# Kernel optimization log

Measured on AMD Instinct MI355X. Metric: run time of the kernel, lower is better.

## Reference

```python
import jax, jax.numpy as jnp
import numpy as np

B, S, H, HEADS = 4, 2048, 512, 8
DK = H // HEADS
LN_EPS = 1e-5
NEG_INF = -1e30


def setup_inputs() -> dict:
    key = jax.random.key(0)
    k = jax.random.split(key, 6)
    x = jax.random.normal(k[0], (B, S, H), dtype=jnp.float32)
    mask = jax.random.randint(k[1], (B, S), 0, 2, dtype=jnp.int32)
    # per-head Q/K/V projection weights stacked: [heads, H, dk]
    Wq = jax.random.normal(k[2], (HEADS, H, DK), dtype=jnp.float32) * 0.05
    Wk = jax.random.normal(k[3], (HEADS, H, DK), dtype=jnp.float32) * 0.05
    Wv = jax.random.normal(k[4], (HEADS, H, DK), dtype=jnp.float32) * 0.05
    # output projection: [heads*dk, H] (y = h @ Wo)
    Wo = jax.random.normal(k[5], (HEADS * DK, H), dtype=jnp.float32) * 0.05
    gamma = jnp.ones((H,), dtype=jnp.float32)
    beta = jnp.zeros((H,), dtype=jnp.float32)
    return {"x": x, "mask": mask, "Wq": Wq, "Wk": Wk, "Wv": Wv,
            "Wo": Wo, "gamma": gamma, "beta": beta}


def reference(x, mask, Wq, Wk, Wv, Wo, gamma, beta):
    # LayerNorm over hidden dim
    mu = jnp.mean(x, axis=-1, keepdims=True)
    var = jnp.mean(jnp.square(x - mu), axis=-1, keepdims=True)
    xn = (x - mu) * jax.lax.rsqrt(var + LN_EPS) * gamma + beta  # [B,S,H]

    mf = mask.astype(jnp.float32)  # [B,S]

    # batched per-head projections (original loops over heads)
    q = jnp.einsum('bsh,nhd->bnsd', xn, Wq)  # [B,heads,S,dk]
    kk = jnp.einsum('bsh,nhd->bnsd', xn, Wk)
    v = jnp.einsum('bsh,nhd->bnsd', xn, Wv)

    scores = jnp.einsum('bnqd,bnkd->bnqk', q, kk) / np.sqrt(DK).astype(np.float32)
    m = mf[:, None, None, :]  # [B,1,1,S] broadcast over query dim
    logits = m * scores + (1.0 - m) * NEG_INF
    probs = jax.nn.softmax(logits, axis=-1)
    attn = jnp.einsum('bnqk,bnkd->bnqd', probs, v)  # [B,heads,S,dk]

    h = attn.transpose(0, 2, 1, 3).reshape(x.shape[0], x.shape[1], HEADS * DK)
    out = h @ Wo + xn          # residual adds post-norm x (as in original)
    out = out * mf[:, :, None]  # zero out masked positions
    return out
```

## Files before the change

kernel.cpp:

```cpp
#include <hip/hip_runtime.h>
#include <hip/hip_bf16.h>
#include <math.h>

#define B_ 4
#define S_ 2048
#define H_ 512
#define HEADS_ 8
#define DK_ 64
#define NROWS_ (B_*S_)
#define LN_EPS_ 1e-5f
#define NEG_INF_ -1e30f
#define QSCALE_ (0.125f * 1.44269504088896f)

typedef short s8v __attribute__((ext_vector_type(8)));
typedef short s4v __attribute__((ext_vector_type(4)));
typedef float f4v __attribute__((ext_vector_type(4)));

typedef __attribute__((address_space(1))) unsigned int gu32_t;
typedef __attribute__((address_space(3))) unsigned int lu32_t;

__device__ __forceinline__ unsigned short f2bf(float f) {
    unsigned int u = __float_as_uint(f);
    u += 0x7FFFu + ((u >> 16) & 1u);
    return (unsigned short)(u >> 16);
}

__device__ __forceinline__ float bf2f(unsigned short u) {
    return __uint_as_float((unsigned int)u << 16);
}

__device__ __forceinline__ s4v pk4bf(float a, float b, float c, float d) {
    union { __hip_bfloat162 h[2]; s4v v; } u;
    u.h[0] = __float22bfloat162_rn(float2{a, b});
    u.h[1] = __float22bfloat162_rn(float2{c, d});
    return u.v;
}

__global__ __launch_bounds__(256) void prep_kernel(
        const float* __restrict__ x, const float* __restrict__ gamma,
        const float* __restrict__ beta, const int* __restrict__ mask,
        const float* __restrict__ Wq, const float* __restrict__ Wk,
        const float* __restrict__ Wv, const float* __restrict__ Wo,
        unsigned short* __restrict__ xnb, float* __restrict__ mb,
        unsigned short* __restrict__ Wt) {
    int bx = blockIdx.x;
    if (bx < 2048) {
        int row  = bx * 4 + (threadIdx.x >> 6);
        int lane = threadIdx.x & 63;
        const float4* xr = (const float4*)(x + (size_t)row * H_ + lane * 8);
        float4 a = xr[0], d = xr[1];
        float s  = (a.x + a.y) + (a.z + a.w) + (d.x + d.y) + (d.z + d.w);
        float ss = (a.x*a.x + a.y*a.y) + (a.z*a.z + a.w*a.w)
                 + (d.x*d.x + d.y*d.y) + (d.z*d.z + d.w*d.w);
        #pragma unroll
        for (int i = 1; i < 64; i <<= 1) {
            s  += __shfl_xor(s, i, 64);
            ss += __shfl_xor(ss, i, 64);
        }
        float mu  = s * (1.f / 512.f);
        float var = ss * (1.f / 512.f) - mu * mu;
        float rstd = rsqrtf(var + LN_EPS_);
        if (lane == 0) mb[row] = mask[row] ? 0.f : NEG_INF_;
        const float4* gp = (const float4*)(gamma + lane * 8);
        const float4* bp = (const float4*)(beta + lane * 8);
        float4 g0 = gp[0], g1 = gp[1], b0 = bp[0], b1 = bp[1];
        float4 y0, y1;
        y0.x = (a.x - mu) * rstd * g0.x + b0.x;
        y0.y = (a.y - mu) * rstd * g0.y + b0.y;
        y0.z = (a.z - mu) * rstd * g0.z + b0.z;
        y0.w = (a.w - mu) * rstd * g0.w + b0.w;
        y1.x = (d.x - mu) * rstd * g1.x + b1.x;
        y1.y = (d.y - mu) * rstd * g1.y + b1.y;
        y1.z = (d.z - mu) * rstd * g1.z + b1.z;
        y1.w = (d.w - mu) * rstd * g1.w + b1.w;
        union { s4v h[2]; s8v v; } pk;
        pk.h[0] = pk4bf(y0.x, y0.y, y0.z, y0.w);
        pk.h[1] = pk4bf(y1.x, y1.y, y1.z, y1.w);
        *(s8v*)(xnb + (size_t)row * H_ + lane * 8) = pk.v;
    } else {
        __shared__ float tile[32][33];
        int wid = bx - 2048;
        const float* src;
        int ld, drow, k0, c0;
        float scale = 1.f;
        if (wid < 768) {
            int z = wid >> 5, rem = wid & 31;
            int cx = rem & 1, ky = rem >> 1;
            k0 = ky * 32; c0 = cx * 32;
            int zw = z >> 3, head = z & 7;
            const float* W = (zw == 0) ? Wq : (zw == 1) ? Wk : Wv;
            if (zw == 0) scale = QSCALE_;
            src = W + (size_t)head * H_ * DK_;
            ld = DK_;
            drow = zw * 512 + head * 64;
        } else {
            int rem = wid - 768;
            int cx = rem & 15, ky = rem >> 4;
            k0 = ky * 32; c0 = cx * 32;
            src = Wo; ld = H_; drow = 1536;
        }
        int tx = threadIdx.x & 31, ty = threadIdx.x >> 5;
        #pragma unroll
        for (int i = 0; i < 4; i++)
            tile[ty * 4 + i][tx] = src[(size_t)(k0 + ty * 4 + i) * ld + c0 + tx];
        __syncthreads();
        #pragma unroll
        for (int i = 0; i < 4; i++) {
            int cc = ty * 4 + i;
            Wt[(size_t)(drow + c0 + cc) * 512 + k0 + tx] = f2bf(tile[tx][cc] * scale);
        }
    }
}

__device__ __forceinline__ void gemm_tile(
        const unsigned short* __restrict__ A,
        const unsigned short* __restrict__ Bt,
        int r0, int j0, f4v acc[4][4]) {
    __shared__ unsigned short As[2 * 128 * 32];
    __shared__ unsigned short Bs[2 * 128 * 32];
    int t = threadIdx.x;
    int wv = t >> 6, L = t & 63, c = L & 15, g = L >> 4;
    int m_base = (wv & 1) * 64, n_base = (wv >> 1) * 64;
    #pragma unroll
    for (int i = 0; i < 4; i++)
        #pragma unroll
        for (int j = 0; j < 4; j++) acc[i][j] = (f4v){0.f, 0.f, 0.f, 0.f};
    for (int k0 = 0; k0 < 512; k0 += 64) {
        __syncthreads();
        #pragma unroll
        for (int half = 0; half < 2; half++) {
            #pragma unroll
            for (int i = 0; i < 2; i++) {
                int u = wv * 128 + i * 64 + L;
                int row = u >> 2, k16 = u & 3;
                __builtin_amdgcn_global_load_lds(
                    (const gu32_t*)(A + (size_t)(r0 + row) * 512 + k0 + half * 32 + k16 * 8),
                    (lu32_t*)(As + half * 4096 + (size_t)(wv * 128 + i * 64) * 8), 16, 0, 0);
                __builtin_amdgcn_global_load_lds(
                    (const gu32_t*)(Bt + (size_t)(j0 + row) * 512 + k0 + half * 32 + k16 * 8),
                    (lu32_t*)(Bs + half * 4096 + (size_t)(wv * 128 + i * 64) * 8), 16, 0, 0);
            }
        }
        __asm__ volatile("s_waitcnt vmcnt(0)" ::: "memory");
        __syncthreads();
        #pragma unroll
        for (int half = 0; half < 2; half++) {
            s8v a[4], b[4];
            #pragma unroll
            for (int i = 0; i < 4; i++)
                a[i] = *(const s8v*)(As + half * 4096 + (size_t)(m_base + i * 16 + c) * 32 + g * 8);
            #pragma unroll
            for (int j = 0; j < 4; j++)
                b[j] = *(const s8v*)(Bs + half * 4096 + (size_t)(n_base + j * 16 + c) * 32 + g * 8);
            #pragma unroll
            for (int i = 0; i < 4; i++)
                #pragma unroll
                for (int j = 0; j < 4; j++)
                    acc[i][j] = __builtin_amdgcn_mfma_f32_16x16x32_bf16(
                        a[i], b[j], acc[i][j], 0, 0, 0);
        }
    }
}

__global__ __launch_bounds__(256) void qkv_gemm(
        const unsigned short* __restrict__ xnb,
        const unsigned short* __restrict__ Wt,
        unsigned short* __restrict__ Qb, unsigned short* __restrict__ Kf,
        unsigned short* __restrict__ Vf) {
    f4v acc[4][4];
    int t = threadIdx.x;
    int wv = t >> 6, L = t & 63, c = L & 15, g = L >> 4;
    int rb = wv & 1, cb = wv >> 1;
    if (blockIdx.x < 8) {
        int m0 = blockIdx.x * 128, n0 = blockIdx.y * 128;
        gemm_tile(Wt, xnb, m0, n0, acc);
        int R0 = m0 + rb * 64;
        int C0 = n0 + cb * 64;
        int hd = (R0 >> 6) & 7;
        int b  = C0 >> 11, srow0 = C0 & 2047;
        size_t bhbase = (size_t)(b * HEADS_ + hd) * S_ * DK_;
        if (R0 < 512) {
            #pragma unroll
            for (int msub = 0; msub < 4; msub++) {
                int dk4 = msub * 16 + g * 4;
                #pragma unroll
                for (int nsub = 0; nsub < 4; nsub++) {
                    int tok = srow0 + nsub * 16 + c;
                    s4v v = pk4bf(acc[msub][nsub][0], acc[msub][nsub][1],
                                  acc[msub][nsub][2], acc[msub][nsub][3]);
                    *(s4v*)(Qb + bhbase + (size_t)tok * DK_ + dk4) = v;
                }
            }
        } else {
            unsigned short* dst = Kf + bhbase + (size_t)(srow0 >> 6) * 4096;
            #pragma unroll
            for (int msub = 0; msub < 4; msub++) {
                int gx = (msub & 1) * 2 + (g >> 1);
                int slotbase = (g & 1) * 4 + (msub >> 1) * 8;
                #pragma unroll
                for (int nsub = 0; nsub < 4; nsub++) {
                    s4v v = pk4bf(acc[msub][nsub][0], acc[msub][nsub][1],
                                  acc[msub][nsub][2], acc[msub][nsub][3]);
                    *(s4v*)(dst + nsub * 1024 + (gx * 16 + c) * 16 + slotbase) = v;
                }
            }
        }
    } else {
        int r0 = blockIdx.y * 128, j0 = 1024 + (blockIdx.x - 8) * 128;
        gemm_tile(xnb, Wt, r0, j0, acc);
        int R0 = r0 + rb * 64;
        int C0 = j0 + cb * 64;
        int hd = (C0 >> 6) & 7;
        int b = R0 >> 11, srow0 = R0 & 2047;
        unsigned short* dst = Vf + (size_t)(b * HEADS_ + hd) * S_ * DK_
                              + (size_t)(srow0 >> 6) * 4096;
        #pragma unroll
        for (int msub = 0; msub < 4; msub++)
            #pragma unroll
            for (int nsub = 0; nsub < 4; nsub++) {
                s4v v = pk4bf(acc[msub][nsub][0], acc[msub][nsub][1],
                              acc[msub][nsub][2], acc[msub][nsub][3]);
                *(s4v*)(dst + nsub * 1024 + (g * 16 + c) * 16 + msub * 4) = v;
            }
    }
}

struct KHalf {
    s8v k0lo, k0hi, k1lo, k1hi;
    float4 mb0, mb1;
};

__global__ __launch_bounds__(256, 3) void attn_kernel(
        const unsigned short* __restrict__ Qb,
        const unsigned short* __restrict__ Kf,
        const unsigned short* __restrict__ Vf,
        const float* __restrict__ mb,
        unsigned short* __restrict__ hb) {
    __shared__ float red[2][64][2][17];

    int wv   = threadIdx.x >> 6;
    int qsub = wv & 1;
    int kp   = wv >> 1;
    int L  = threadIdx.x & 63;
    int c  = L & 15;
    int g  = L >> 4;

    unsigned wgid = blockIdx.x + blockIdx.y * 32u;
    unsigned xcd  = wgid & 7u;
    unsigned idx  = wgid >> 3;
    int bh = (int)(xcd + (idx >> 5) * 8u);
    int qt = (int)(idx & 31u);
    int b  = bh >> 3, n = bh & 7;
    int q0 = qt * 64 + qsub * 32;

    const unsigned short* Qbase = Qb + (size_t)bh * S_ * DK_;
    const unsigned short* Kp = Kf + (size_t)bh * S_ * DK_ + (size_t)kp * 16 * 4096 + L * 16;
    const unsigned short* Vp = Vf + (size_t)bh * S_ * DK_ + (size_t)kp * 16 * 4096 + L * 16;
    const float* mbrow = mb + b * S_ + kp * 1024;

    s8v qfA0 = *(const s8v*)(Qbase + (size_t)(q0 + c) * DK_ + g * 8);
    s8v qfA1 = *(const s8v*)(Qbase + (size_t)(q0 + c) * DK_ + 32 + g * 8);
    s8v qfB0 = *(const s8v*)(Qbase + (size_t)(q0 + 16 + c) * DK_ + g * 8);
    s8v qfB1 = *(const s8v*)(Qbase + (size_t)(q0 + 16 + c) * DK_ + 32 + g * 8);

    f4v accA[4], accB[4];
    #pragma unroll
    for (int i = 0; i < 4; i++) {
        accA[i] = (f4v){0.f, 0.f, 0.f, 0.f};
        accB[i] = (f4v){0.f, 0.f, 0.f, 0.f};
    }
    float lacA[4] = {0.f, 0.f, 0.f, 0.f};
    float lacB[4] = {0.f, 0.f, 0.f, 0.f};

    auto load_kh = [&](int kb, int h, KHalf& d) {
        const unsigned short* Kn = Kp + (size_t)kb * 4096;
        d.k0lo = *(const s8v*)(Kn + (h * 2 + 0) * 1024);
        d.k0hi = *(const s8v*)(Kn + (h * 2 + 0) * 1024 + 8);
        d.k1lo = *(const s8v*)(Kn + (h * 2 + 1) * 1024);
        d.k1hi = *(const s8v*)(Kn + (h * 2 + 1) * 1024 + 8);
        d.mb0  = *(const float4*)(mbrow + kb * 64 + h * 32 + g * 4);
        d.mb1  = *(const float4*)(mbrow + kb * 64 + h * 32 + 16 + g * 4);
    };

    auto compute_half = [&](const KHalf& d, int kb, int h) {
        const unsigned short* Vn = Vp + (size_t)kb * 4096;
        s8v vv[4];
        #pragma unroll
        for (int ds = 0; ds < 4; ds++)
            vv[ds] = *(const s8v*)(Vn + ds * 1024 + h * 8);
        f4v bias0 = (f4v){d.mb0.x, d.mb0.y, d.mb0.z, d.mb0.w};
        f4v bias1 = (f4v){d.mb1.x, d.mb1.y, d.mb1.z, d.mb1.w};
        f4v sA0 = bias0, sA1 = bias1, sB0 = bias0, sB1 = bias1;
        sA0 = __builtin_amdgcn_mfma_f32_16x16x32_bf16(d.k0lo, qfA0, sA0, 0, 0, 0);
        sA0 = __builtin_amdgcn_mfma_f32_16x16x32_bf16(d.k0hi, qfA1, sA0, 0, 0, 0);
        sA1 = __builtin_amdgcn_mfma_f32_16x16x32_bf16(d.k1lo, qfA0, sA1, 0, 0, 0);
        sA1 = __builtin_amdgcn_mfma_f32_16x16x32_bf16(d.k1hi, qfA1, sA1, 0, 0, 0);
        sB0 = __builtin_amdgcn_mfma_f32_16x16x32_bf16(d.k0lo, qfB0, sB0, 0, 0, 0);
        sB0 = __builtin_amdgcn_mfma_f32_16x16x32_bf16(d.k0hi, qfB1, sB0, 0, 0, 0);
        sB1 = __builtin_amdgcn_mfma_f32_16x16x32_bf16(d.k1lo, qfB0, sB1, 0, 0, 0);
        sB1 = __builtin_amdgcn_mfma_f32_16x16x32_bf16(d.k1hi, qfB1, sB1, 0, 0, 0);
        float pA0[4], pA1[4], pB0[4], pB1[4];
        #pragma unroll
        for (int r = 0; r < 4; r++) {
            pA0[r] = __builtin_amdgcn_exp2f(sA0[r]);
            pA1[r] = __builtin_amdgcn_exp2f(sA1[r]);
            pB0[r] = __builtin_amdgcn_exp2f(sB0[r]);
            pB1[r] = __builtin_amdgcn_exp2f(sB1[r]);
            lacA[r] += pA0[r] + pA1[r];
            lacB[r] += pB0[r] + pB1[r];
        }
        s4v pfA0 = pk4bf(pA0[0], pA0[1], pA0[2], pA0[3]);
        s4v pfA1 = pk4bf(pA1[0], pA1[1], pA1[2], pA1[3]);
        s4v pfB0 = pk4bf(pB0[0], pB0[1], pB0[2], pB0[3]);
        s4v pfB1 = pk4bf(pB1[0], pB1[1], pB1[2], pB1[3]);
        #pragma unroll
        for (int ds = 0; ds < 4; ds++) {
            s4v v0 = __builtin_shufflevector(vv[ds], vv[ds], 0, 1, 2, 3);
            s4v v1 = __builtin_shufflevector(vv[ds], vv[ds], 4, 5, 6, 7);
            accA[ds] = __builtin_amdgcn_mfma_f32_16x16x16bf16_1k(v0, pfA0, accA[ds], 0, 0, 0);
            accA[ds] = __builtin_amdgcn_mfma_f32_16x16x16bf16_1k(v1, pfA1, accA[ds], 0, 0, 0);
            accB[ds] = __builtin_amdgcn_mfma_f32_16x16x16bf16_1k(v0, pfB0, accB[ds], 0, 0, 0);
            accB[ds] = __builtin_amdgcn_mfma_f32_16x16x16bf16_1k(v1, pfB1, accB[ds], 0, 0, 0);
        }
    };

    KHalf ha, hb2;
    load_kh(0, 0, ha);
    for (int kb = 0; kb < 16; kb++) {
        load_kh(kb, 1, hb2);
        compute_half(ha, kb, 0);
        int kbn = (kb < 15) ? kb + 1 : 15;
        load_kh(kbn, 0, ha);
        compute_half(hb2, kb, 1);
    }

    float lA = (lacA[0] + lacA[1]) + (lacA[2] + lacA[3]);
    float lB = (lacB[0] + lacB[1]) + (lacB[2] + lacB[3]);
    lA += __shfl_xor(lA, 16, 64);
    lA += __shfl_xor(lA, 32, 64);
    lB += __shfl_xor(lB, 16, 64);
    lB += __shfl_xor(lB, 32, 64);

    if (kp == 1) {
        #pragma unroll
        for (int d = 0; d < 4; d++) {
            #pragma unroll
            for (int r = 0; r < 4; r++) {
                red[qsub][L][0][d * 4 + r] = accA[d][r];
                red[qsub][L][1][d * 4 + r] = accB[d][r];
            }
        }
        red[qsub][L][0][16] = lA;
        red[qsub][L][1][16] = lB;
    }
    __syncthreads();
    if (kp == 0) {
        const float* srcA = &red[qsub][L][0][0];
        const float* srcB = &red[qsub][L][1][0];
        float invA = 1.f / (lA + srcA[16]);
        float invB = 1.f / (lB + srcB[16]);
        unsigned short* hpA = hb + (size_t)(b * S_ + q0 + c) * H_ + n * DK_ + g * 4;
        unsigned short* hpB = hpA + (size_t)16 * H_;
        #pragma unroll
        for (int ds = 0; ds < 4; ds++) {
            s4v oA = pk4bf((accA[ds][0] + srcA[ds * 4 + 0]) * invA,
                           (accA[ds][1] + srcA[ds * 4 + 1]) * invA,
                           (accA[ds][2] + srcA[ds * 4 + 2]) * invA,
                           (accA[ds][3] + srcA[ds * 4 + 3]) * invA);
            *(s4v*)(hpA + ds * 16) = oA;
            s4v oB = pk4bf((accB[ds][0] + srcB[ds * 4 + 0]) * invB,
                           (accB[ds][1] + srcB[ds * 4 + 1]) * invB,
                           (accB[ds][2] + srcB[ds * 4 + 2]) * invB,
                           (accB[ds][3] + srcB[ds * 4 + 3]) * invB);
            *(s4v*)(hpB + ds * 16) = oB;
        }
    }
}

__global__ __launch_bounds__(256) void out_gemm(
        const unsigned short* __restrict__ hb,
        const unsigned short* __restrict__ Wot,
        const unsigned short* __restrict__ xnb, const int* __restrict__ mask,
        float* __restrict__ out) {
    f4v acc[4][4];
    int r0 = blockIdx.y * 128, j0 = blockIdx.x * 128;
    gemm_tile(hb, Wot, r0, j0, acc);
    int t = threadIdx.x;
    int wv = t >> 6, L = t & 63, c = L & 15, g = L >> 4;
    int mrow = r0 + (wv & 1) * 64 + g * 4;
    int ncol = j0 + (wv >> 1) * 64 + c;
    #pragma unroll
    for (int msub = 0; msub < 4; msub++) {
        #pragma unroll
        for (int rr = 0; rr < 4; rr++) {
            int row = mrow + msub * 16 + rr;
            float mf = (float)mask[row];
            #pragma unroll
            for (int nsub = 0; nsub < 4; nsub++) {
                int col = ncol + nsub * 16;
                size_t o = (size_t)row * H_ + col;
                out[o] = (acc[msub][nsub][rr] + bf2f(xnb[o])) * mf;
            }
        }
    }
}

extern "C" void kernel_launch(void* const* d_in, const int* in_sizes, int n_in,
                              void* d_out, int out_size, void* d_ws, size_t ws_size,
                              hipStream_t stream) {
    const float* x     = (const float*)d_in[0];
    const int*   mask  = (const int*)d_in[1];
    const float* Wq    = (const float*)d_in[2];
    const float* Wk    = (const float*)d_in[3];
    const float* Wv    = (const float*)d_in[4];
    const float* Wo    = (const float*)d_in[5];
    const float* gamma = (const float*)d_in[6];
    const float* beta  = (const float*)d_in[7];
    float* out = (float*)d_out;

    size_t nelem = (size_t)NROWS_ * H_;
    char* ws = (char*)d_ws;
    unsigned short* xnb = (unsigned short*)ws; ws += nelem * 2;
    unsigned short* hb  = (unsigned short*)ws; ws += nelem * 2;
    unsigned short* Qb  = (unsigned short*)ws; ws += nelem * 2;
    unsigned short* Kf  = (unsigned short*)ws; ws += nelem * 2;
    unsigned short* Vf  = (unsigned short*)ws; ws += nelem * 2;
    unsigned short* Wt  = (unsigned short*)ws; ws += (size_t)2048 * 512 * 2;
    float*          mbp = (float*)ws;

    prep_kernel<<<3072, 256, 0, stream>>>(
        x, gamma, beta, mask, Wq, Wk, Wv, Wo, xnb, mbp, Wt);
    qkv_gemm<<<dim3(12, 64), 256, 0, stream>>>(xnb, Wt, Qb, Kf, Vf);
    attn_kernel<<<dim3(S_ / 64, B_ * HEADS_), 256, 0, stream>>>(
        Qb, Kf, Vf, mbp, hb);
    out_gemm<<<dim3(4, 64), 256, 0, stream>>>(
        hb, Wt + (size_t)1536 * 512, xnb, mask, out);
}
```

Before: 184.0 us.

## Double-buffer GEMM tile loads to overlap global-to-LDS copies with MFMA

The shared GEMM tile routine now splits K into 32-wide steps and uses two LDS buffers. The next step's global-to-LDS load is issued before computing on the current buffer, and a partial vmcnt wait keeps the new loads in flight. This aims to hide memory latency behind MFMA work. In exchange it uses twice as many barriers per K step, relies on raw s_barrier with hand-counted vmcnt, and makes each compute step smaller.

```diff
diff --git a/kernel.cpp b/kernel.cpp
--- a/kernel.cpp
+++ b/kernel.cpp
@@ -125,41 +125,50 @@
     for (int i = 0; i < 4; i++)
         #pragma unroll
         for (int j = 0; j < 4; j++) acc[i][j] = (f4v){0.f, 0.f, 0.f, 0.f};
-    for (int k0 = 0; k0 < 512; k0 += 64) {
-        __syncthreads();
-        #pragma unroll
-        for (int half = 0; half < 2; half++) {
-            #pragma unroll
-            for (int i = 0; i < 2; i++) {
-                int u = wv * 128 + i * 64 + L;
-                int row = u >> 2, k16 = u & 3;
-                __builtin_amdgcn_global_load_lds(
-                    (const gu32_t*)(A + (size_t)(r0 + row) * 512 + k0 + half * 32 + k16 * 8),
-                    (lu32_t*)(As + half * 4096 + (size_t)(wv * 128 + i * 64) * 8), 16, 0, 0);
-                __builtin_amdgcn_global_load_lds(
-                    (const gu32_t*)(Bt + (size_t)(j0 + row) * 512 + k0 + half * 32 + k16 * 8),
-                    (lu32_t*)(Bs + half * 4096 + (size_t)(wv * 128 + i * 64) * 8), 16, 0, 0);
-            }
-        }
-        __asm__ volatile("s_waitcnt vmcnt(0)" ::: "memory");
-        __syncthreads();
-        #pragma unroll
-        for (int half = 0; half < 2; half++) {
-            s8v a[4], b[4];
-            #pragma unroll
-            for (int i = 0; i < 4; i++)
-                a[i] = *(const s8v*)(As + half * 4096 + (size_t)(m_base + i * 16 + c) * 32 + g * 8);
+
+    auto stage = [&](int buf, int k0) {
+        #pragma unroll
+        for (int i = 0; i < 2; i++) {
+            int uu = wv * 128 + i * 64 + L;
+            int row = uu >> 2, k16 = uu & 3;
+            __builtin_amdgcn_global_load_lds(
+                (const gu32_t*)(A + (size_t)(r0 + row) * 512 + k0 + k16 * 8),
+                (lu32_t*)(As + buf * 4096 + (size_t)(wv * 128 + i * 64) * 8), 16, 0, 0);
+            __builtin_amdgcn_global_load_lds(
+                (const gu32_t*)(Bt + (size_t)(j0 + row) * 512 + k0 + k16 * 8),
+                (lu32_t*)(Bs + buf * 4096 + (size_t)(wv * 128 + i * 64) * 8), 16, 0, 0);
+        }
+    };
+
+    auto compute = [&](int buf) {
+        s8v a[4], b[4];
+        #pragma unroll
+        for (int i = 0; i < 4; i++)
+            a[i] = *(const s8v*)(As + buf * 4096 + (size_t)(m_base + i * 16 + c) * 32 + g * 8);
+        #pragma unroll
+        for (int j = 0; j < 4; j++)
+            b[j] = *(const s8v*)(Bs + buf * 4096 + (size_t)(n_base + j * 16 + c) * 32 + g * 8);
+        #pragma unroll
+        for (int i = 0; i < 4; i++)
             #pragma unroll
             for (int j = 0; j < 4; j++)
-                b[j] = *(const s8v*)(Bs + half * 4096 + (size_t)(n_base + j * 16 + c) * 32 + g * 8);
-            #pragma unroll
-            for (int i = 0; i < 4; i++)
-                #pragma unroll
-                for (int j = 0; j < 4; j++)
-                    acc[i][j] = __builtin_amdgcn_mfma_f32_16x16x32_bf16(
-                        a[i], b[j], acc[i][j], 0, 0, 0);
-        }
-    }
+                acc[i][j] = __builtin_amdgcn_mfma_f32_16x16x32_bf16(
+                    a[i], b[j], acc[i][j], 0, 0, 0);
+    };
+
+    stage(0, 0);
+    int cur = 0;
+    for (int s = 0; s < 15; ++s) {
+        stage(cur ^ 1, (s + 1) * 32);
+        __asm__ volatile("s_waitcnt vmcnt(4)" ::: "memory");
+        __builtin_amdgcn_s_barrier();
+        compute(cur);
+        __builtin_amdgcn_s_barrier();
+        cur ^= 1;
+    }
+    __asm__ volatile("s_waitcnt vmcnt(0)" ::: "memory");
+    __builtin_amdgcn_s_barrier();
+    compute(cur);
 }
 
 __global__ __launch_bounds__(256) void qkv_gemm(
```

Result: no change. 180.4 us (-1.9%).
